# Kernel optimization log

Measured on AMD Instinct MI355X. Metric: run time of the kernel, lower is better.

The kernel has to match this reference:

```python
import jax, jax.numpy as jnp
import numpy as np

NEG_SLOPE = 0.2

def gat_conv(x, src, dst, W, a_src, a_dst, b, num_nodes, concat):
    # PyG GATConv (add_self_loops already applied to src/dst).
    H, C = a_src.shape
    h = (x @ W).reshape(-1, H, C)                      # [N,H,C]
    s = jnp.einsum('nhc,hc->nh', h, a_src)             # per-node src score
    d = jnp.einsum('nhc,hc->nh', h, a_dst)             # per-node dst score
    e = jax.nn.leaky_relu(s[src] + d[dst], NEG_SLOPE)  # [E,H]
    emax = jax.lax.stop_gradient(
        jax.ops.segment_max(e, dst, num_segments=num_nodes))  # [N,H]
    ex = jnp.exp(e - emax[dst])
    denom = jax.ops.segment_sum(ex, dst, num_segments=num_nodes)
    alpha = ex / denom[dst]                            # segment softmax over in-edges
    msg = h[src] * alpha[:, :, None]                   # [E,H,C]
    out = jax.ops.segment_sum(msg, dst, num_segments=num_nodes)
    out = out.reshape(num_nodes, H * C) if concat else out.mean(axis=1)
    return out + b

def setup_inputs() -> dict:
    key = jax.random.key(0)
    ks = jax.random.split(key, 20)
    N, E, F = 50000, 400000, 256
    x = jax.random.normal(ks[0], (N, F), dtype=jnp.float32)
    edge_index = jax.random.randint(ks[1], (2, E), 0, N, dtype=jnp.int64)
    def p(k, shape):
        return (jax.random.normal(k, shape, dtype=jnp.float32) * 0.1)
    inp = {'x': x, 'edge_index': edge_index}
    # conv1: 256 -> 8x32 ; conv2: 256 -> 4x32 ; conv3: 128 -> 2x32 ; conv4: 64 -> 1x32
    dims = [(256, 8, 32), (256, 4, 32), (128, 2, 32), (64, 1, 32)]
    ki = 2
    for i, (fin, H, C) in enumerate(dims, start=1):
        inp[f'W{i}'] = p(ks[ki], (fin, H * C)); ki += 1
        inp[f'a_src{i}'] = p(ks[ki], (H, C)); ki += 1
        inp[f'a_dst{i}'] = p(ks[ki], (H, C)); ki += 1
        bdim = H * C if i < 4 else C
        inp[f'b{i}'] = jnp.zeros((bdim,), dtype=jnp.float32)
    return inp

def reference(x, edge_index, W1, a_src1, a_dst1, b1, W2, a_src2, a_dst2, b2,
              W3, a_src3, a_dst3, b3, W4, a_src4, a_dst4, b4):
    N = x.shape[0]
    loops = jnp.arange(N, dtype=edge_index.dtype)
    src = jnp.concatenate([edge_index[0], loops])
    dst = jnp.concatenate([edge_index[1], loops])
    h = jax.nn.elu(gat_conv(x, src, dst, W1, a_src1, a_dst1, b1, N, True))
    h = jax.nn.elu(gat_conv(h, src, dst, W2, a_src2, a_dst2, b2, N, True))
    h = gat_conv(h, src, dst, W3, a_src3, a_dst3, b3, N, True)
    h = jax.nn.elu(h)
    h = gat_conv(h, src, dst, W4, a_src4, a_dst4, b4, N, False)
    return jax.nn.log_softmax(h, axis=1)
```

## Files before the change

kernel.cpp:

```cpp
#include <hip/hip_runtime.h>
#include <hip/hip_bf16.h>

#define LRELU_SLOPE 0.2f

typedef __attribute__((ext_vector_type(8))) short short8;
typedef __attribute__((ext_vector_type(4))) float f32x4;

__device__ __forceinline__ unsigned short bf16r(float f) {
    unsigned int u = __builtin_bit_cast(unsigned int, f);
    u += 0x7fffu + ((u >> 16) & 1u);
    return (unsigned short)(u >> 16);
}
__device__ __forceinline__ float bf2f(unsigned short u) {
    return __builtin_bit_cast(float, (unsigned int)u << 16);
}


#define WTOT 108544

__global__ void k_pre(const float* __restrict__ Wa, const float* __restrict__ Wb,
                      const float* __restrict__ Wc, const float* __restrict__ Wd,
                      unsigned short* __restrict__ Ta, unsigned short* __restrict__ Tb,
                      unsigned short* __restrict__ Tc, unsigned short* __restrict__ Td,
                      const int* __restrict__ ei, int* __restrict__ cnt, int E, int N) {
    int gid = blockIdx.x * blockDim.x + threadIdx.x;
    if (gid < WTOT) {
        int id = gid;
        const float* W; unsigned short* T; int K, Nc;
        if (id < 65536)       { W = Wa; T = Ta; K = 256; Nc = 256; }
        else if (id < 98304)  { id -= 65536;  W = Wb; T = Tb; K = 256; Nc = 128; }
        else if (id < 106496) { id -= 98304;  W = Wc; T = Tc; K = 128; Nc = 64; }
        else                  { id -= 106496; W = Wd; T = Td; K = 64;  Nc = 32; }
        int n = id / K, k = id % K;
        T[id] = bf16r(W[(long)k * Nc + n]);
        return;
    }
    int e = gid - WTOT;
    if (e >= E + N) return;
    int dst = (e < E) ? ei[E + e] : (e - E);
    atomicAdd(&cnt[dst], 1);
}


__global__ void k_scan_blk(const int* __restrict__ cnt, int* __restrict__ offs,
                           int* __restrict__ bsum, int N) {
    __shared__ int temp[1024];
    int t = threadIdx.x;
    int gi = blockIdx.x * 1024 + t;
    int v = (gi < N) ? cnt[gi] : 0;
    temp[t] = v;
    __syncthreads();
    for (int o = 1; o < 1024; o <<= 1) {
        int x = (t >= o) ? temp[t - o] : 0;
        __syncthreads();
        temp[t] += x;
        __syncthreads();
    }
    if (gi < N) offs[gi] = temp[t] - v;
    if (t == 1023) bsum[blockIdx.x] = temp[1023];
}

__global__ void k_scan(const int* __restrict__ cnt, int* __restrict__ offs, int N) {
    __shared__ int temp[1024];
    __shared__ int carry_s;
    int t = threadIdx.x;
    if (t == 0) carry_s = 0;
    __syncthreads();
    for (int base = 0; base < N; base += 1024) {
        int v = (base + t < N) ? cnt[base + t] : 0;
        temp[t] = v;
        __syncthreads();
        for (int o = 1; o < 1024; o <<= 1) {
            int x = (t >= o) ? temp[t - o] : 0;
            __syncthreads();
            temp[t] += x;
            __syncthreads();
        }
        int incl = temp[t];
        int carry = carry_s;
        if (base + t < N) offs[base + t] = carry + incl - v;
        __syncthreads();
        if (t == 1023) carry_s = carry + temp[1023];
        __syncthreads();
    }
    if (t == 0) offs[N] = carry_s;
}

__global__ void k_scan_add(int* __restrict__ offs, const int* __restrict__ bpre,
                           int* __restrict__ wp, int N, int nb) {
    int gi = blockIdx.x * blockDim.x + threadIdx.x;
    if (gi < N) {
        int v = offs[gi] + bpre[gi >> 10];
        offs[gi] = v;
        wp[gi] = v;
    } else if (gi == N) {
        offs[N] = bpre[nb];
    }
}

__global__ void k_scatter(const int* __restrict__ ei, int* __restrict__ wp,
                          int* __restrict__ adj, int E, int N) {
    int e = blockIdx.x * blockDim.x + threadIdx.x;
    if (e >= E + N) return;
    int srcn = (e < E) ? ei[e] : (e - E);
    int dst  = (e < E) ? ei[E + e] : (e - E);
    int pos = atomicAdd(&wp[dst], 1);
    adj[pos] = srcn;
}


template<int BN, int KT, bool F32A>
__global__ __launch_bounds__(256) void k_mgemm(const void* __restrict__ Ain,
                                               const unsigned short* __restrict__ WT,
                                               unsigned short* __restrict__ Cb,
                                               const float* __restrict__ a_src,
                                               const float* __restrict__ a_dst,
                                               float* __restrict__ sbuf,
                                               float* __restrict__ dbuf,
                                               int M, int Nc, int H) {
    constexpr int KITER = KT / 32;
    constexpr int KS  = KT + 8;
    constexpr int NBF = BN / 16;
    constexpr int CPR = BN / 32;
    constexpr int SP  = BN + 8;
    constexpr int STAGE = BN * KS;
    constexpr int EPIL  = 64 * SP;
    constexpr int LBSZ  = STAGE > EPIL ? STAGE : EPIL;
    __shared__ __align__(16) unsigned short LB[LBSZ];

    int t = threadIdx.x;
    int wv = t >> 6, l = t & 63;
    int row_in = l & 15, quad = l >> 4;
    int bm = blockIdx.y * 64, bn = blockIdx.x * BN;

    int grA = min(bm + wv * 16 + row_in, M - 1);
    const float* Af = (const float*)Ain;
    const unsigned short* Ab = (const unsigned short*)Ain;
    float4 af0[KITER], af1[KITER];
    short8 areg[KITER];
    if constexpr (F32A) {
#pragma unroll
        for (int ki = 0; ki < KITER; ++ki) {
            const float4* p = (const float4*)&Af[(long)grA * KT + ki * 32 + quad * 8];
            af0[ki] = p[0];
            af1[ki] = p[1];
        }
    } else {
#pragma unroll
        for (int ki = 0; ki < KITER; ++ki)
            areg[ki] = *(const short8*)&Ab[(long)grA * KT + ki * 32 + quad * 8];
    }

    constexpr int PER = BN * (KT / 8) / 256;
#pragma unroll
    for (int i = 0; i < PER; ++i) {
        int ch = t + i * 256;
        int col = ch / (KT / 8);
        int kc  = ch % (KT / 8);
        int gcol = min(bn + col, Nc - 1);
        *(short8*)&LB[col * KS + kc * 8] = *(const short8*)&WT[(long)gcol * KT + kc * 8];
    }
    __syncthreads();

    f32x4 acc[NBF];
#pragma unroll
    for (int j = 0; j < NBF; ++j) acc[j] = (f32x4){0.f, 0.f, 0.f, 0.f};

#pragma unroll
    for (int ki = 0; ki < KITER; ++ki) {
        short8 av;
        if constexpr (F32A) {
            float4 f0 = af0[ki], f1 = af1[ki];
            av[0] = (short)bf16r(f0.x); av[1] = (short)bf16r(f0.y);
            av[2] = (short)bf16r(f0.z); av[3] = (short)bf16r(f0.w);
            av[4] = (short)bf16r(f1.x); av[5] = (short)bf16r(f1.y);
            av[6] = (short)bf16r(f1.z); av[7] = (short)bf16r(f1.w);
        } else {
            av = areg[ki];
        }
#pragma unroll
        for (int f = 0; f < NBF; ++f) {
            short8 bv = *(const short8*)&LB[(f * 16 + row_in) * KS + ki * 32 + quad * 8];
            acc[f] = __builtin_amdgcn_mfma_f32_16x16x32_bf16(av, bv, acc[f], 0, 0, 0);
        }
    }
    __syncthreads();

#pragma unroll
    for (int r = 0; r < 4; ++r)
#pragma unroll
        for (int f = 0; f < NBF; ++f)
            LB[(wv * 16 + quad * 4 + r) * SP + f * 16 + row_in] = bf16r(acc[f][r]);
    __syncthreads();

    int rr = t / CPR, cc = t % CPR;
    if (rr < 64) {
        int grow = bm + rr;
        int colb = bn + cc * 32;
        if (grow < M && colb < Nc) {
            const unsigned short* ep = &LB[rr * SP + cc * 32];
            short8 v0 = *(const short8*)(ep);
            short8 v1 = *(const short8*)(ep + 8);
            short8 v2 = *(const short8*)(ep + 16);
            short8 v3 = *(const short8*)(ep + 24);
            unsigned short* cp = &Cb[(long)grow * Nc + colb];
            *(short8*)(cp)      = v0;
            *(short8*)(cp + 8)  = v1;
            *(short8*)(cp + 16) = v2;
            *(short8*)(cp + 24) = v3;
            int hd = colb >> 5;
            const float* ap = a_src + hd * 32;
            const float* dp = a_dst + hd * 32;
            float ss = 0.f, dd = 0.f;
#pragma unroll
            for (int u = 0; u < 8; ++u) {
                float va = bf2f((unsigned short)v0[u]); ss += va * ap[u];      dd += va * dp[u];
                float vb = bf2f((unsigned short)v1[u]); ss += vb * ap[8 + u];  dd += vb * dp[8 + u];
                float vc = bf2f((unsigned short)v2[u]); ss += vc * ap[16 + u]; dd += vc * dp[16 + u];
                float vd = bf2f((unsigned short)v3[u]); ss += vd * ap[24 + u]; dd += vd * dp[24 + u];
            }
            sbuf[(long)grow * H + hd] = ss;
            dbuf[(long)grow * H + hd] = dd;
        }
    }
}


template<int ACT>
__global__ void k_aggf(const unsigned short* __restrict__ h, const float* __restrict__ s,
                       const float* __restrict__ dsc, const int* __restrict__ offs,
                       const int* __restrict__ adj, const float* __restrict__ bias,
                       unsigned short* __restrict__ out16, float* __restrict__ out32,
                       int N, int H) {
    const int C8 = 4;
    long tid = (long)blockIdx.x * blockDim.x + threadIdx.x;
    int HC8 = H * C8;
    if (tid >= (long)N * HC8) return;
    int c8 = (int)(tid % C8);
    int hh = (int)((tid / C8) % H);
    int n  = (int)(tid / HC8);
    int beg = offs[n], end = offs[n + 1];
    float dn = dsc[n * H + hh];
    int HC = HC8 * 8;
    int coff = hh * 32 + c8 * 8;

    float denom = 0.f;
    float acc[8];
#pragma unroll
    for (int u = 0; u < 8; ++u) acc[u] = 0.f;

    for (int j = beg; j < end; ++j) {
        int sn = adj[j];
        float e = s[sn * H + hh] + dn;
        e = e > 0.f ? e : LRELU_SLOPE * e;
        float w = __expf(fminf(e, 80.f));
        short8 hv = *(const short8*)(h + (size_t)sn * HC + coff);
        denom += w;
#pragma unroll
        for (int u = 0; u < 8; ++u)
            acc[u] += w * bf2f((unsigned short)hv[u]);
    }

    float inv = 1.0f / denom;
    float o[8];
#pragma unroll
    for (int u = 0; u < 8; ++u) o[u] = acc[u] * inv + bias[coff + u];

    if (ACT == 1) {
        short8 pk;
#pragma unroll
        for (int u = 0; u < 8; ++u) {
            float v = o[u] > 0.f ? o[u] : (__expf(o[u]) - 1.f);
            pk[u] = (short)bf16r(v);
        }
        *(short8*)(out16 + tid * 8) = pk;
    } else {
        float m = o[0];
#pragma unroll
        for (int u = 1; u < 8; ++u) m = fmaxf(m, o[u]);
        m = fmaxf(m, __shfl_xor(m, 1));
        m = fmaxf(m, __shfl_xor(m, 2));
        float ssum = 0.f;
#pragma unroll
        for (int u = 0; u < 8; ++u) ssum += __expf(o[u] - m);
        ssum += __shfl_xor(ssum, 1);
        ssum += __shfl_xor(ssum, 2);
        float lse = m + __logf(ssum);
        float4 lo = {o[0] - lse, o[1] - lse, o[2] - lse, o[3] - lse};
        float4 hi = {o[4] - lse, o[5] - lse, o[6] - lse, o[7] - lse};
        *(float4*)(out32 + tid * 8)     = lo;
        *(float4*)(out32 + tid * 8 + 4) = hi;
    }
}


static inline size_t align_up(size_t x) { return (x + 255) & ~(size_t)255; }

extern "C" void kernel_launch(void* const* d_in, const int* in_sizes, int n_in,
                              void* d_out, int out_size, void* d_ws, size_t ws_size,
                              hipStream_t stream) {
    const float* x   = (const float*)d_in[0];
    const int*   ei  = (const int*)d_in[1];

    const int N = in_sizes[0] / 256;
    const int E = in_sizes[1] / 2;
    const int ET = E + N;
    const int NB = (N + 1023) / 1024;

    size_t off = 0;
    char* ws = (char*)d_ws;
    auto take = [&](size_t bytes) { char* p = ws + off; off += align_up(bytes); return p; };
    int*   offs  = (int*)take((size_t)(N + 1) * 4);
    int*   wp    = (int*)take((size_t)N * 4);
    int*   adj   = (int*)take((size_t)ET * 4);
    int*   bsum  = (int*)take((size_t)(NB + 1) * 4);
    int*   bpre  = (int*)take((size_t)(NB + 1) * 4);
    float* sbuf  = (float*)take((size_t)N * 8 * 4);
    float* dbuf  = (float*)take((size_t)N * 8 * 4);
    unsigned short* Xb = (unsigned short*)take((size_t)N * 256 * 2);
    unsigned short* Yb = (unsigned short*)take((size_t)N * 256 * 2);
    unsigned short* WT0 = (unsigned short*)take((size_t)256 * 256 * 2);
    unsigned short* WT1 = (unsigned short*)take((size_t)256 * 128 * 2);
    unsigned short* WT2 = (unsigned short*)take((size_t)128 * 64 * 2);
    unsigned short* WT3 = (unsigned short*)take((size_t)64 * 32 * 2);
    (void)ws_size;

    hipMemsetAsync(wp, 0, (size_t)N * 4, stream);
    {
        long tot = WTOT + ET;
        k_pre<<<(int)((tot + 255) / 256), 256, 0, stream>>>(
            (const float*)d_in[2], (const float*)d_in[6], (const float*)d_in[10],
            (const float*)d_in[14], WT0, WT1, WT2, WT3, ei, wp, E, N);
        k_scan_blk<<<NB, 1024, 0, stream>>>(wp, offs, bsum, N);
        k_scan<<<1, 1024, 0, stream>>>(bsum, bpre, NB);
        k_scan_add<<<(N + 256) / 256, 256, 0, stream>>>(offs, bpre, wp, N, NB);
        k_scatter<<<(ET + 255) / 256, 256, 0, stream>>>(ei, wp, adj, E, N);
    }

    const float* as_[4] = {(const float*)d_in[3], (const float*)d_in[7],
                           (const float*)d_in[11], (const float*)d_in[15]};
    const float* ad_[4] = {(const float*)d_in[4], (const float*)d_in[8],
                           (const float*)d_in[12], (const float*)d_in[16]};
    const float* b_[4]  = {(const float*)d_in[5], (const float*)d_in[9],
                           (const float*)d_in[13], (const float*)d_in[17]};
    int H_[4] = {8, 4, 2, 1};

    int gy = (N + 63) / 64;
    for (int li = 0; li < 4; ++li) {
        int H = H_[li];
        int HC = H * 32;

        if (li == 0) {
            k_mgemm<64, 256, true><<<dim3(4, gy), 256, 0, stream>>>(
                x, WT0, Yb, as_[0], ad_[0], sbuf, dbuf, N, 256, H);
        } else if (li == 1) {
            k_mgemm<64, 256, false><<<dim3(2, gy), 256, 0, stream>>>(
                Xb, WT1, Yb, as_[1], ad_[1], sbuf, dbuf, N, 128, H);
        } else if (li == 2) {
            k_mgemm<64, 128, false><<<dim3(1, gy), 256, 0, stream>>>(
                Xb, WT2, Yb, as_[2], ad_[2], sbuf, dbuf, N, 64, H);
        } else {
            k_mgemm<32, 64, false><<<dim3(1, gy), 256, 0, stream>>>(
                Xb, WT3, Yb, as_[3], ad_[3], sbuf, dbuf, N, 32, H);
        }
        {
            long total = (long)N * H * 4;
            int nb = (int)((total + 255) / 256);
            if (li < 3)
                k_aggf<1><<<nb, 256, 0, stream>>>(Yb, sbuf, dbuf, offs, adj, b_[li],
                                                  Xb, nullptr, N, H);
            else
                k_aggf<0><<<nb, 256, 0, stream>>>(Yb, sbuf, dbuf, offs, adj, b_[li],
                                                  nullptr, (float*)d_out, N, H);
        }
    }
}
```

Before: 340.2 us.

## Compute all output column tiles per block to reuse A rows across N

The GEMM kernel now loops over all column tiles inside one block instead of launching a separate block per column tile. Each block loads and converts its 64 A rows once and reuses them for every output column tile, with W tiles staged through shared memory one after another. This removes the repeated reads of A (notably the fp32 input in layer 1) and the repeated bf16 conversion. In exchange there are fewer blocks, more accumulator registers, and extra barriers between W tile loads, with no overlap between loading W and computing.

```diff
diff --git a/kernel.cpp b/kernel.cpp
--- a/kernel.cpp
+++ b/kernel.cpp
@@ -109,7 +109,7 @@
 }
 
 
-template<int BN, int KT, bool F32A>
+template<int BN, int CT, int KT, bool F32A>
 __global__ __launch_bounds__(256) void k_mgemm(const void* __restrict__ Ain,
                                                const unsigned short* __restrict__ WT,
                                                unsigned short* __restrict__ Cb,
@@ -117,12 +117,13 @@
                                                const float* __restrict__ a_dst,
                                                float* __restrict__ sbuf,
                                                float* __restrict__ dbuf,
-                                               int M, int Nc, int H) {
+                                               int M, int H) {
+    constexpr int NC    = BN * CT;
     constexpr int KITER = KT / 32;
-    constexpr int KS  = KT + 8;
-    constexpr int NBF = BN / 16;
-    constexpr int CPR = BN / 32;
-    constexpr int SP  = BN + 8;
+    constexpr int KS    = KT + 8;
+    constexpr int NBF   = BN / 16;
+    constexpr int CPR   = NC / 32;
+    constexpr int SP    = NC + 8;
     constexpr int STAGE = BN * KS;
     constexpr int EPIL  = 64 * SP;
     constexpr int LBSZ  = STAGE > EPIL ? STAGE : EPIL;
@@ -131,57 +132,63 @@
     int t = threadIdx.x;
     int wv = t >> 6, l = t & 63;
     int row_in = l & 15, quad = l >> 4;
-    int bm = blockIdx.y * 64, bn = blockIdx.x * BN;
+    int bm = blockIdx.x * 64;
 
     int grA = min(bm + wv * 16 + row_in, M - 1);
-    const float* Af = (const float*)Ain;
-    const unsigned short* Ab = (const unsigned short*)Ain;
-    float4 af0[KITER], af1[KITER];
     short8 areg[KITER];
     if constexpr (F32A) {
+        const float* Af = (const float*)Ain;
+        float4 af0[KITER], af1[KITER];
 #pragma unroll
         for (int ki = 0; ki < KITER; ++ki) {
             const float4* p = (const float4*)&Af[(long)grA * KT + ki * 32 + quad * 8];
             af0[ki] = p[0];
             af1[ki] = p[1];
         }
-    } else {
-#pragma unroll
-        for (int ki = 0; ki < KITER; ++ki)
-            areg[ki] = *(const short8*)&Ab[(long)grA * KT + ki * 32 + quad * 8];
-    }
-
-    constexpr int PER = BN * (KT / 8) / 256;
-#pragma unroll
-    for (int i = 0; i < PER; ++i) {
-        int ch = t + i * 256;
-        int col = ch / (KT / 8);
-        int kc  = ch % (KT / 8);
-        int gcol = min(bn + col, Nc - 1);
-        *(short8*)&LB[col * KS + kc * 8] = *(const short8*)&WT[(long)gcol * KT + kc * 8];
-    }
-    __syncthreads();
-
-    f32x4 acc[NBF];
-#pragma unroll
-    for (int j = 0; j < NBF; ++j) acc[j] = (f32x4){0.f, 0.f, 0.f, 0.f};
-
-#pragma unroll
-    for (int ki = 0; ki < KITER; ++ki) {
-        short8 av;
-        if constexpr (F32A) {
+#pragma unroll
+        for (int ki = 0; ki < KITER; ++ki) {
             float4 f0 = af0[ki], f1 = af1[ki];
+            short8 av;
             av[0] = (short)bf16r(f0.x); av[1] = (short)bf16r(f0.y);
             av[2] = (short)bf16r(f0.z); av[3] = (short)bf16r(f0.w);
             av[4] = (short)bf16r(f1.x); av[5] = (short)bf16r(f1.y);
             av[6] = (short)bf16r(f1.z); av[7] = (short)bf16r(f1.w);
-        } else {
-            av = areg[ki];
-        }
-#pragma unroll
-        for (int f = 0; f < NBF; ++f) {
-            short8 bv = *(const short8*)&LB[(f * 16 + row_in) * KS + ki * 32 + quad * 8];
-            acc[f] = __builtin_amdgcn_mfma_f32_16x16x32_bf16(av, bv, acc[f], 0, 0, 0);
+            areg[ki] = av;
+        }
+    } else {
+        const unsigned short* Ab = (const unsigned short*)Ain;
+#pragma unroll
+        for (int ki = 0; ki < KITER; ++ki)
+            areg[ki] = *(const short8*)&Ab[(long)grA * KT + ki * 32 + quad * 8];
+    }
+
+    f32x4 acc[CT][NBF];
+#pragma unroll
+    for (int c = 0; c < CT; ++c)
+#pragma unroll
+        for (int j = 0; j < NBF; ++j) acc[c][j] = (f32x4){0.f, 0.f, 0.f, 0.f};
+
+    constexpr int PER = BN * (KT / 8) / 256;
+#pragma unroll
+    for (int ct = 0; ct < CT; ++ct) {
+        if (ct > 0) __syncthreads();
+#pragma unroll
+        for (int i = 0; i < PER; ++i) {
+            int ch = t + i * 256;
+            int col = ch / (KT / 8);
+            int kc  = ch % (KT / 8);
+            *(short8*)&LB[col * KS + kc * 8] =
+                *(const short8*)&WT[(long)(ct * BN + col) * KT + kc * 8];
+        }
+        __syncthreads();
+#pragma unroll
+        for (int ki = 0; ki < KITER; ++ki) {
+            short8 av = areg[ki];
+#pragma unroll
+            for (int f = 0; f < NBF; ++f) {
+                short8 bv = *(const short8*)&LB[(f * 16 + row_in) * KS + ki * 32 + quad * 8];
+                acc[ct][f] = __builtin_amdgcn_mfma_f32_16x16x32_bf16(av, bv, acc[ct][f], 0, 0, 0);
+            }
         }
     }
     __syncthreads();
@@ -189,28 +196,30 @@
 #pragma unroll
     for (int r = 0; r < 4; ++r)
 #pragma unroll
-        for (int f = 0; f < NBF; ++f)
-            LB[(wv * 16 + quad * 4 + r) * SP + f * 16 + row_in] = bf16r(acc[f][r]);
+        for (int ct = 0; ct < CT; ++ct)
+#pragma unroll
+            for (int f = 0; f < NBF; ++f)
+                LB[(wv * 16 + quad * 4 + r) * SP + ct * BN + f * 16 + row_in] =
+                    bf16r(acc[ct][f][r]);
     __syncthreads();
 
-    int rr = t / CPR, cc = t % CPR;
-    if (rr < 64) {
+    constexpr int TOT = 64 * CPR;
+    for (int ch = t; ch < TOT; ch += 256) {
+        int rr = ch / CPR, cc = ch % CPR;
         int grow = bm + rr;
-        int colb = bn + cc * 32;
-        if (grow < M && colb < Nc) {
+        if (grow < M) {
             const unsigned short* ep = &LB[rr * SP + cc * 32];
             short8 v0 = *(const short8*)(ep);
             short8 v1 = *(const short8*)(ep + 8);
             short8 v2 = *(const short8*)(ep + 16);
             short8 v3 = *(const short8*)(ep + 24);
-            unsigned short* cp = &Cb[(long)grow * Nc + colb];
+            unsigned short* cp = &Cb[(long)grow * NC + cc * 32];
             *(short8*)(cp)      = v0;
             *(short8*)(cp + 8)  = v1;
             *(short8*)(cp + 16) = v2;
             *(short8*)(cp + 24) = v3;
-            int hd = colb >> 5;
-            const float* ap = a_src + hd * 32;
-            const float* dp = a_dst + hd * 32;
+            const float* ap = a_src + cc * 32;
+            const float* dp = a_dst + cc * 32;
             float ss = 0.f, dd = 0.f;
 #pragma unroll
             for (int u = 0; u < 8; ++u) {
@@ -219,8 +228,8 @@
                 float vc = bf2f((unsigned short)v2[u]); ss += vc * ap[16 + u]; dd += vc * dp[16 + u];
                 float vd = bf2f((unsigned short)v3[u]); ss += vd * ap[24 + u]; dd += vd * dp[24 + u];
             }
-            sbuf[(long)grow * H + hd] = ss;
-            dbuf[(long)grow * H + hd] = dd;
+            sbuf[(long)grow * H + cc] = ss;
+            dbuf[(long)grow * H + cc] = dd;
         }
     }
 }
@@ -348,20 +357,19 @@
     int gy = (N + 63) / 64;
     for (int li = 0; li < 4; ++li) {
         int H = H_[li];
-        int HC = H * 32;
 
         if (li == 0) {
-            k_mgemm<64, 256, true><<<dim3(4, gy), 256, 0, stream>>>(
-                x, WT0, Yb, as_[0], ad_[0], sbuf, dbuf, N, 256, H);
+            k_mgemm<64, 4, 256, true><<<gy, 256, 0, stream>>>(
+                x, WT0, Yb, as_[0], ad_[0], sbuf, dbuf, N, H);
         } else if (li == 1) {
-            k_mgemm<64, 256, false><<<dim3(2, gy), 256, 0, stream>>>(
-                Xb, WT1, Yb, as_[1], ad_[1], sbuf, dbuf, N, 128, H);
+            k_mgemm<64, 2, 256, false><<<gy, 256, 0, stream>>>(
+                Xb, WT1, Yb, as_[1], ad_[1], sbuf, dbuf, N, H);
         } else if (li == 2) {
-            k_mgemm<64, 128, false><<<dim3(1, gy), 256, 0, stream>>>(
-                Xb, WT2, Yb, as_[2], ad_[2], sbuf, dbuf, N, 64, H);
+            k_mgemm<64, 1, 128, false><<<gy, 256, 0, stream>>>(
+                Xb, WT2, Yb, as_[2], ad_[2], sbuf, dbuf, N, H);
         } else {
-            k_mgemm<32, 64, false><<<dim3(1, gy), 256, 0, stream>>>(
-                Xb, WT3, Yb, as_[3], ad_[3], sbuf, dbuf, N, 32, H);
+            k_mgemm<32, 1, 64, false><<<gy, 256, 0, stream>>>(
+                Xb, WT3, Yb, as_[3], ad_[3], sbuf, dbuf, N, H);
         }
         {
             long total = (long)N * H * 4;
```

Result: slower. 358.6 us (+5.4%).
